# Optimization experiments

Measured on AMD Instinct MI355X. Metric: run time of the kernel, lower is better.

The kernel has to match this reference:

```python
import jax, jax.numpy as jnp
import numpy as np

BETA = 1.0
EPS_MU = 1e-6
EPS_LOG = 1e-8
D_DIM = 2048
M_EVENTS = 16384
T_HORIZON = 100


def setup_inputs() -> dict:
    key = jax.random.key(0)
    k1, k2 = jax.random.split(key)
    # sorted event times in [0, T_HORIZON)
    t_events = jnp.sort(jax.random.uniform(k1, (M_EVENTS,), jnp.float32) * T_HORIZON)
    marks = jax.random.randint(k2, (M_EVENTS,), 0, D_DIM)  # int marks in {0..D-1}
    # learned params, init exactly as in torch module
    log_mu = jnp.full((D_DIM,), -3.0, jnp.float32)
    log_alpha = jnp.full((D_DIM, D_DIM), -4.0, jnp.float32)
    return {
        "t_events": t_events,
        "marks": marks,
        "T_max": T_HORIZON,
        "log_mu": log_mu,
        "log_alpha": log_alpha,
    }


def _loglik(t_events, log_mu, log_alpha, marks, T_max, beta=BETA):
    mu = jax.nn.softplus(log_mu) + EPS_MU          # [D]
    alpha = jax.nn.softplus(log_alpha)             # [D, D]
    D = mu.shape[0]
    # dt[0] = 0 so the first step leaves S (= zeros) untouched, matching the
    # torch loop which skips decay at n == 0.
    dt = jnp.concatenate([jnp.zeros((1,), t_events.dtype), jnp.diff(t_events)])  # [M]

    def step(S, xs):
        dt_n, d = xs
        S = jnp.exp(-beta * dt_n) * S              # exponential decay of state [D]
        lam_d = mu[d] + alpha[d] @ S               # intensity at event's mark
        S = S.at[d].add(1.0)                       # self-excitation bump
        return S, jnp.log(lam_d + EPS_LOG)

    _, log_lams = jax.lax.scan(step, jnp.zeros((D,), mu.dtype), (dt, marks))

    # compensator integral term
    T = jnp.asarray(T_max, t_events.dtype)
    one_minus_exp = 1.0 - jnp.exp(-beta * (T - t_events))          # [M]
    contrib = jax.ops.segment_sum(one_minus_exp, marks, num_segments=D)  # [D]
    integral = mu * T + alpha @ (contrib / beta)                   # [D]
    return log_lams.sum() - integral.sum()


def reference(t_events, marks, T_max, log_mu, log_alpha):
    return _loglik(t_events, log_mu, log_alpha, marks, T_max)
```

## Files before the change

kernel.cpp:

```cpp
#include <hip/hip_runtime.h>
#include <math.h>

#define D_DIM 2048
#define M_EV  16384
#define LCH   32
#define CCH   (M_EV / LCH)
#define SEG   32
#define NSEG  (CCH / SEG)
#define BETA  1.0f
#define NSH   8

__device__ __forceinline__ float softplus_f(float x){
  float e = __expf(-fabsf(x));
  return fmaxf(x, 0.0f) + __logf(1.0f + e);
}

__device__ __forceinline__ unsigned short f2bf(float f){
  unsigned b = __float_as_uint(f);
  return (unsigned short)((b + 0x7FFFu + ((b >> 16) & 1u)) >> 16);
}
__device__ __forceinline__ float bf2f(unsigned short u){
  return __uint_as_float(((unsigned)u) << 16);
}

__device__ __forceinline__ float decode_T(const void* p){
  unsigned bits = *(const unsigned*)p;
  float fv = __uint_as_float(bits);
  return (fv >= 1e-3f && fv <= 1e7f) ? fv : (float)(int)bits;
}

__device__ __forceinline__ float wave_red(float v){
  #pragma unroll
  for (int o = 32; o > 0; o >>= 1) v += __shfl_down(v, o);
  return v;
}

__global__ __launch_bounds__(256) void k_prep(
    const float* __restrict__ t, const int* __restrict__ m,
    const float* __restrict__ log_mu,
    float* __restrict__ muw, float* __restrict__ SL,
    float* __restrict__ dchunk, float* __restrict__ cumdec,
    float* __restrict__ Aseg, float* __restrict__ colsum,
    float* __restrict__ acc)
{
  __shared__ float Srow[8 * D_DIM];
  const int b = blockIdx.x, tid = threadIdx.x;
  if (b < 8){
    int j = b*256 + tid;
    float v = softplus_f(log_mu[j]) + 1e-6f;
    muw[j] = v;
    float s = wave_red(v);
    if ((tid & 63) == 0) Srow[tid >> 6] = s;
    __syncthreads();
    if (tid == 0) acc[8 + b] = (Srow[0]+Srow[1]) + (Srow[2]+Srow[3]);
  } else if (b < 72){
    float4* S4 = (float4*)Srow;
    const float4 z = make_float4(0.f,0.f,0.f,0.f);
    #pragma unroll
    for (int k = 0; k < 16; ++k) S4[k*256 + tid] = z;
    __syncthreads();
    const int i = (b-8)*256 + tid;
    const int c = i >> 5;
    if (c < CCH - 1){
      float tn = t[(c+1)*LCH];
      atomicAdd(&Srow[(tid >> 5)*D_DIM + m[i]], __expf(-BETA * (tn - t[i])));
    }
    __syncthreads();
    float4* G4 = (float4*)(SL + (size_t)(b-8) * (8*D_DIM));
    #pragma unroll
    for (int k = 0; k < 16; ++k) G4[k*256 + tid] = S4[k*256 + tid];
  } else {
    int c = (b-72)*256 + tid;
    float tc = t[c*LCH];
    dchunk[c] = (c < CCH-1) ? __expf(-BETA * (t[(c+1)*LCH] - tc)) : 1.0f;
    int s0c = (c >> 5) << 5;
    cumdec[c] = __expf(-BETA * (tc - t[s0c*LCH]));
    float4* C4 = (float4*)colsum;
    const float4 z = make_float4(0.f,0.f,0.f,0.f);
    int q0 = ((b-72)*256 + tid) * 8;
    #pragma unroll
    for (int k = 0; k < 8; ++k) C4[q0 + k] = z;
    if (b == 72 && tid < NSEG){
      int s = tid;
      Aseg[s] = (s < NSEG-1)
        ? __expf(-BETA * (t[(s+1)*SEG*LCH] - t[s*SEG*LCH])) : 1.0f;
    }
    if (b == 73 && tid < 4) acc[tid] = 0.f;
  }
}

__global__ __launch_bounds__(256) void k_scan_alpha(
    float* __restrict__ SL, const float* __restrict__ dchunk,
    float* __restrict__ Carry, const float* __restrict__ la,
    unsigned short* __restrict__ sA, float* __restrict__ colsum)
{
  const int b = blockIdx.x, tid = threadIdx.x;
  if (b < 128){
    const int seg = b >> 3, jb = b & 7;
    const int j = jb*256 + tid;
    const int c0 = seg * SEG;
    const size_t base = (size_t)c0 * D_DIM + j;
    float u = 0.f;
    float cur[4], nxt[4];
    #pragma unroll
    for (int q = 0; q < 4; ++q) cur[q] = SL[base + (size_t)q * D_DIM];
    for (int g = 0; g < SEG; g += 4){
      #pragma unroll
      for (int q = 0; q < 4; ++q)
        nxt[q] = (g+4 < SEG) ? SL[base + (size_t)(g+4+q) * D_DIM] : 0.f;
      #pragma unroll
      for (int q = 0; q < 4; ++q){
        int c = c0 + g + q;
        float l = cur[q];
        SL[(size_t)c * D_DIM + j] = u;
        u = fmaf(dchunk[c], u, l);
      }
      #pragma unroll
      for (int q = 0; q < 4; ++q) cur[q] = nxt[q];
    }
    Carry[(size_t)seg * D_DIM + j] = u;
    return;
  }
  const int nthreads = 512*256;
  int atid = (b-128)*256 + tid;
  const float4* la4 = (const float4*)la;
  ushort4* sA4 = (ushort4*)sA;
  float p0=0.f, p1=0.f, p2=0.f, p3=0.f;
  #pragma unroll
  for (int u = 0; u < 8; ++u){
    int i4 = atid + u * nthreads;
    float4 x = la4[i4];
    float4 sp;
    sp.x = softplus_f(x.x); sp.y = softplus_f(x.y);
    sp.z = softplus_f(x.z); sp.w = softplus_f(x.w);
    ushort4 h;
    h.x = f2bf(sp.x); h.y = f2bf(sp.y); h.z = f2bf(sp.z); h.w = f2bf(sp.w);
    sA4[i4] = h;
    p0 += sp.x; p1 += sp.y; p2 += sp.z; p3 += sp.w;
  }
  const int col = (atid * 4) & (D_DIM - 1);
  float* cs = colsum + (size_t)(b & 7) * D_DIM;
  atomicAdd(&cs[col+0], p0);
  atomicAdd(&cs[col+1], p1);
  atomicAdd(&cs[col+2], p2);
  atomicAdd(&cs[col+3], p3);
}

__global__ __launch_bounds__(512) void k_events(
    const float* __restrict__ t, const int* __restrict__ m,
    const unsigned short* __restrict__ sA, const float* __restrict__ muw,
    const float* __restrict__ SL, const float* __restrict__ Carry,
    const float* __restrict__ Aseg, const float* __restrict__ cumdec,
    const float* __restrict__ colsum, float* __restrict__ acc,
    const void* Tp, float* __restrict__ out){
  __shared__ float S0[D_DIM];
  __shared__ float tl[LCH];
  __shared__ int   ml[LCH];
  __shared__ float wred[8];
  const int tid = threadIdx.x;
  const int c = blockIdx.x;
  const int seg = c >> 5;
  const float cd = cumdec[c];

  {
    const float4 sv = *(const float4*)(SL + (size_t)c * D_DIM + tid*4);
    float4 e = {0.f, 0.f, 0.f, 0.f};
    float wgt = 1.f;
    for (int s = seg - 1; s >= 0; --s){
      const float4 cr = *(const float4*)(Carry + (size_t)s * D_DIM + tid*4);
      e.x = fmaf(cr.x, wgt, e.x); e.y = fmaf(cr.y, wgt, e.y);
      e.z = fmaf(cr.z, wgt, e.z); e.w = fmaf(cr.w, wgt, e.w);
      wgt *= Aseg[s];
    }
    float4 s;
    s.x = fmaf(e.x, cd, sv.x); s.y = fmaf(e.y, cd, sv.y);
    s.z = fmaf(e.z, cd, sv.z); s.w = fmaf(e.w, cd, sv.w);
    *(float4*)&S0[tid*4] = s;
  }
  if (tid < LCH){
    ml[tid] = m[c*LCH + tid];
    tl[tid] = t[c*LCH + tid];
  }
  __syncthreads();

  if (tid < 64){
    float v = 0.f;
    if (tid < 32){
      int d = ml[tid];
      float cstot = 0.f;
      #pragma unroll
      for (int s = 0; s < NSH; ++s) cstot += colsum[s*D_DIM + d];
      float T = decode_T(Tp);
      v = cstot * (1.0f - __expf(-BETA * (T - tl[tid])));
    }
    v = wave_red(v);
    if (tid == 0) atomicAdd(&acc[1], v);
  }

  const int l = tid & 63, w = tid >> 6;
  const int l4 = l * 4;

  float4 s0[8];
  #pragma unroll
  for (int u = 0; u < 8; ++u) s0[u] = *(const float4*)&S0[u*256 + l4];

  const float t0 = tl[0];
  float lgw = 0.f;
  #pragma unroll
  for (int q = 0; q < 4; ++q){
    const int k = w*4 + q;
    const int d = ml[k];
    const unsigned short* row = sA + (size_t)d * D_DIM;
    float p = 0.f;
    #pragma unroll
    for (int u = 0; u < 8; ++u){
      ushort4 a = *(const ushort4*)(row + u*256 + l4);
      p = fmaf(bf2f(a.x), s0[u].x, p);
      p = fmaf(bf2f(a.y), s0[u].y, p);
      p = fmaf(bf2f(a.z), s0[u].z, p);
      p = fmaf(bf2f(a.w), s0[u].w, p);
    }
    const float tk = tl[k];
    float g = 0.f;
    if (l < k) g = bf2f(row[ml[l]]) * __expf(tl[l] - tk);
    p = fmaf(p, __expf(t0 - tk), g);
    float v = wave_red(p);
    if (l == 0) lgw += __logf(muw[d] + v + 1e-8f);
  }
  if (l == 0) wred[w] = lgw;
  __syncthreads();
  if (tid == 0){
    float lg = ((wred[0]+wred[1])+(wred[2]+wred[3]))
             + ((wred[4]+wred[5])+(wred[6]+wred[7]));
    atomicAdd(&acc[0], lg);
    __threadfence();
    unsigned old = atomicAdd((unsigned*)&acc[3], 1u);
    if (old == CCH - 1){
      float a0 = atomicAdd(&acc[0], 0.0f);
      float a1 = atomicAdd(&acc[1], 0.0f);
      float musum = 0.f;
      #pragma unroll
      for (int j = 8; j < 16; ++j) musum += atomicAdd(&acc[j], 0.0f);
      float T = decode_T(Tp);
      out[0] = a0 - (T * musum + a1 * (1.0f / BETA));
    }
  }
}

extern "C" void kernel_launch(void* const* d_in, const int* in_sizes, int n_in,
                              void* d_out, int out_size, void* d_ws, size_t ws_size,
                              hipStream_t stream) {
  const float* t_events  = (const float*)d_in[0];
  const int*   marks     = (const int*)  d_in[1];
  const void*  Tp        =               d_in[2];
  const float* log_mu    = (const float*)d_in[3];
  const float* log_alpha = (const float*)d_in[4];
  float* out = (float*)d_out;

  float* ws      = (float*)d_ws;
  float* SL      = ws;
  float* Carry   = SL + (size_t)CCH * D_DIM;
  float* muw     = Carry + (size_t)NSEG * D_DIM;
  float* dchunk  = muw + D_DIM;
  float* cumdec  = dchunk + CCH;
  float* Aseg    = cumdec + CCH;
  float* colsum  = Aseg + NSEG;
  float* acc     = colsum + (size_t)NSH * D_DIM;
  unsigned short* sA = (unsigned short*)(acc + 16);

  k_prep      <<<74, 256, 0, stream>>>(t_events, marks, log_mu, muw, SL,
                                       dchunk, cumdec, Aseg, colsum, acc);
  k_scan_alpha<<<640, 256, 0, stream>>>(SL, dchunk, Carry, log_alpha, sA, colsum);
  k_events    <<<CCH, 512, 0, stream>>>(t_events, marks, sA, muw, SL, Carry,
                                        Aseg, cumdec, colsum, acc, Tp, out);
}
```

Baseline: 131.8 us.

## Compute compensator via per-mark contrib dotted with alpha instead of column sums

The compensator term sum_d sum_j alpha[d][j]*contrib[j] used to be computed by atomically accumulating alpha column sums into sharded buffers and then gathering them per event in the events kernel. Now extra prep blocks build per-mark contrib partials in shared memory. The alpha-softplus blocks then dot each softplus value with the matching contrib entry and reduce per block into a single accumulator. This removes four global atomics per thread, the colsum zeroing, and the gather/reduction work in every events block, at the cost of one block-level atomic and a few extra prep blocks. It also relies on the column index (atid & 511) matching across all unrolled iterations.

```diff
diff --git a/kernel.cpp b/kernel.cpp
--- a/kernel.cpp
+++ b/kernel.cpp
@@ -8,7 +8,7 @@
 #define SEG   32
 #define NSEG  (CCH / SEG)
 #define BETA  1.0f
-#define NSH   8
+#define CPB   8
 
 __device__ __forceinline__ float softplus_f(float x){
   float e = __expf(-fabsf(x));
@@ -37,10 +37,10 @@
 
 __global__ __launch_bounds__(256) void k_prep(
     const float* __restrict__ t, const int* __restrict__ m,
-    const float* __restrict__ log_mu,
+    const float* __restrict__ log_mu, const void* Tp,
     float* __restrict__ muw, float* __restrict__ SL,
     float* __restrict__ dchunk, float* __restrict__ cumdec,
-    float* __restrict__ Aseg, float* __restrict__ colsum,
+    float* __restrict__ Aseg, float* __restrict__ Cpart,
     float* __restrict__ acc)
 {
   __shared__ float Srow[8 * D_DIM];
@@ -69,30 +69,42 @@
     float4* G4 = (float4*)(SL + (size_t)(b-8) * (8*D_DIM));
     #pragma unroll
     for (int k = 0; k < 16; ++k) G4[k*256 + tid] = S4[k*256 + tid];
+  } else if (b < 72 + CPB){
+    float* Cl = Srow;
+    float4* Cl4 = (float4*)Cl;
+    const float4 z = make_float4(0.f,0.f,0.f,0.f);
+    Cl4[tid*2] = z; Cl4[tid*2 + 1] = z;
+    __syncthreads();
+    const float T = decode_T(Tp);
+    #pragma unroll
+    for (int k = 0; k < 8; ++k){
+      int i = (b-72)*2048 + k*256 + tid;
+      atomicAdd(&Cl[m[i]], 1.0f - __expf(-BETA * (T - t[i])));
+    }
+    __syncthreads();
+    float4* Cp4 = (float4*)(Cpart + (size_t)(b-72) * D_DIM);
+    Cp4[tid*2]     = Cl4[tid*2];
+    Cp4[tid*2 + 1] = Cl4[tid*2 + 1];
   } else {
-    int c = (b-72)*256 + tid;
+    int c = (b-80)*256 + tid;
     float tc = t[c*LCH];
     dchunk[c] = (c < CCH-1) ? __expf(-BETA * (t[(c+1)*LCH] - tc)) : 1.0f;
     int s0c = (c >> 5) << 5;
     cumdec[c] = __expf(-BETA * (tc - t[s0c*LCH]));
-    float4* C4 = (float4*)colsum;
-    const float4 z = make_float4(0.f,0.f,0.f,0.f);
-    int q0 = ((b-72)*256 + tid) * 8;
-    #pragma unroll
-    for (int k = 0; k < 8; ++k) C4[q0 + k] = z;
-    if (b == 72 && tid < NSEG){
+    if (b == 80 && tid < NSEG){
       int s = tid;
       Aseg[s] = (s < NSEG-1)
         ? __expf(-BETA * (t[(s+1)*SEG*LCH] - t[s*SEG*LCH])) : 1.0f;
     }
-    if (b == 73 && tid < 4) acc[tid] = 0.f;
+    if (b == 81 && tid < 8) acc[tid] = 0.f;
   }
 }
 
 __global__ __launch_bounds__(256) void k_scan_alpha(
     float* __restrict__ SL, const float* __restrict__ dchunk,
     float* __restrict__ Carry, const float* __restrict__ la,
-    unsigned short* __restrict__ sA, float* __restrict__ colsum)
+    const float* __restrict__ Cpart, unsigned short* __restrict__ sA,
+    float* __restrict__ acc)
 {
   const int b = blockIdx.x, tid = threadIdx.x;
   if (b < 128){
@@ -123,9 +135,17 @@
   }
   const int nthreads = 512*256;
   int atid = (b-128)*256 + tid;
+  const float4* Cp4 = (const float4*)Cpart;
+  const int cq = atid & 511;
+  float4 cb = make_float4(0.f,0.f,0.f,0.f);
+  #pragma unroll
+  for (int r = 0; r < CPB; ++r){
+    float4 v = Cp4[r*512 + cq];
+    cb.x += v.x; cb.y += v.y; cb.z += v.z; cb.w += v.w;
+  }
   const float4* la4 = (const float4*)la;
   ushort4* sA4 = (ushort4*)sA;
-  float p0=0.f, p1=0.f, p2=0.f, p3=0.f;
+  float p = 0.f;
   #pragma unroll
   for (int u = 0; u < 8; ++u){
     int i4 = atid + u * nthreads;
@@ -136,14 +156,17 @@
     ushort4 h;
     h.x = f2bf(sp.x); h.y = f2bf(sp.y); h.z = f2bf(sp.z); h.w = f2bf(sp.w);
     sA4[i4] = h;
-    p0 += sp.x; p1 += sp.y; p2 += sp.z; p3 += sp.w;
-  }
-  const int col = (atid * 4) & (D_DIM - 1);
-  float* cs = colsum + (size_t)(b & 7) * D_DIM;
-  atomicAdd(&cs[col+0], p0);
-  atomicAdd(&cs[col+1], p1);
-  atomicAdd(&cs[col+2], p2);
-  atomicAdd(&cs[col+3], p3);
+    p = fmaf(sp.x, cb.x, p);
+    p = fmaf(sp.y, cb.y, p);
+    p = fmaf(sp.z, cb.z, p);
+    p = fmaf(sp.w, cb.w, p);
+  }
+  __shared__ float red[4];
+  float w = wave_red(p);
+  int lane = tid & 63, wid = tid >> 6;
+  if (lane == 0) red[wid] = w;
+  __syncthreads();
+  if (tid == 0) atomicAdd(&acc[1], red[0]+red[1]+red[2]+red[3]);
 }
 
 __global__ __launch_bounds__(512) void k_events(
@@ -151,8 +174,7 @@
     const unsigned short* __restrict__ sA, const float* __restrict__ muw,
     const float* __restrict__ SL, const float* __restrict__ Carry,
     const float* __restrict__ Aseg, const float* __restrict__ cumdec,
-    const float* __restrict__ colsum, float* __restrict__ acc,
-    const void* Tp, float* __restrict__ out){
+    float* __restrict__ acc, const void* Tp, float* __restrict__ out){
   __shared__ float S0[D_DIM];
   __shared__ float tl[LCH];
   __shared__ int   ml[LCH];
@@ -182,20 +204,6 @@
     tl[tid] = t[c*LCH + tid];
   }
   __syncthreads();
-
-  if (tid < 64){
-    float v = 0.f;
-    if (tid < 32){
-      int d = ml[tid];
-      float cstot = 0.f;
-      #pragma unroll
-      for (int s = 0; s < NSH; ++s) cstot += colsum[s*D_DIM + d];
-      float T = decode_T(Tp);
-      v = cstot * (1.0f - __expf(-BETA * (T - tl[tid])));
-    }
-    v = wave_red(v);
-    if (tid == 0) atomicAdd(&acc[1], v);
-  }
 
   const int l = tid & 63, w = tid >> 6;
   const int l4 = l * 4;
@@ -264,13 +272,14 @@
   float* dchunk  = muw + D_DIM;
   float* cumdec  = dchunk + CCH;
   float* Aseg    = cumdec + CCH;
-  float* colsum  = Aseg + NSEG;
-  float* acc     = colsum + (size_t)NSH * D_DIM;
+  float* Cpart   = Aseg + NSEG;
+  float* acc     = Cpart + (size_t)CPB * D_DIM;
   unsigned short* sA = (unsigned short*)(acc + 16);
 
-  k_prep      <<<74, 256, 0, stream>>>(t_events, marks, log_mu, muw, SL,
-                                       dchunk, cumdec, Aseg, colsum, acc);
-  k_scan_alpha<<<640, 256, 0, stream>>>(SL, dchunk, Carry, log_alpha, sA, colsum);
+  k_prep      <<<82, 256, 0, stream>>>(t_events, marks, log_mu, Tp, muw, SL,
+                                       dchunk, cumdec, Aseg, Cpart, acc);
+  k_scan_alpha<<<640, 256, 0, stream>>>(SL, dchunk, Carry, log_alpha, Cpart,
+                                        sA, acc);
   k_events    <<<CCH, 512, 0, stream>>>(t_events, marks, sA, muw, SL, Carry,
-                                        Aseg, cumdec, colsum, acc, Tp, out);
-}
+                                        Aseg, cumdec, acc, Tp, out);
+}
```

Result: faster. 112.5 us (-14.6%).
